# Kernel tuning notes

Measured on AMD Instinct MI355X. Metric: run time of the kernel, lower is better.

The kernel has to match this reference:

```python
import jax, jax.numpy as jnp
import numpy as np

G = 20000          # num_genes
B = 256            # batch_size
NNZ = 640000       # sparse adjacency nonzeros (avg degree 32)
K = 2              # PPR iterations
ALPHA = 0.1
NUM_CLASS = 33


def _spmm(rows, cols, vals, x):
    # y = A @ x with A sparse COO [G, G], x dense [G, B]
    return jax.ops.segment_sum(vals[:, None] * x[cols], rows, num_segments=G)


def setup_inputs() -> dict:
    key = jax.random.key(0)
    ks = jax.random.split(key, 18)
    inp = {
        "x_sample": jax.random.normal(ks[0], (B * G,), jnp.float32),
        "x_TF": jax.random.normal(ks[1], (B * G,), jnp.float32),
        "adj_rows": jax.random.randint(ks[2], (NNZ,), 0, G, jnp.int32),
        "adj_cols": jax.random.randint(ks[3], (NNZ,), 0, G, jnp.int32),
        "adj_vals": jax.random.uniform(ks[4], (NNZ,), jnp.float32) / 32.0,
        "adjT_rows": jax.random.randint(ks[5], (NNZ,), 0, G, jnp.int32),
        "adjT_cols": jax.random.randint(ks[6], (NNZ,), 0, G, jnp.int32),
        "adjT_vals": jax.random.uniform(ks[7], (NNZ,), jnp.float32) / 32.0,
        # learned scalar affine params (torch.rand(1))
        "emb_mut": jax.random.uniform(ks[8], (1,), jnp.float32),
        "bias_mut": jax.random.uniform(ks[9], (1,), jnp.float32),
        "emb_exp": jax.random.uniform(ks[10], (1,), jnp.float32),
        "bias_exp": jax.random.uniform(ks[11], (1,), jnp.float32),
        # MLP params (torch Linear layout: W [out, in])
        "W1": jax.random.normal(ks[12], (1024, G), jnp.float32) * (1.0 / np.sqrt(G)),
        "b1": jnp.zeros((1024,), jnp.float32),
        "W2": jax.random.normal(ks[13], (128, 1024), jnp.float32) * (1.0 / 32.0),
        "b2": jnp.zeros((128,), jnp.float32),
        "W3": jax.random.normal(ks[14], (NUM_CLASS, 128), jnp.float32) * (1.0 / np.sqrt(128.0)),
        "b3": jnp.zeros((NUM_CLASS,), jnp.float32),
    }
    return inp


def reference(x_sample, x_TF, adj_rows, adj_cols, adj_vals,
              adjT_rows, adjT_cols, adjT_vals,
              emb_mut, bias_mut, emb_exp, bias_exp,
              W1, b1, W2, b2, W3, b3):
    # scalar affine embedding + relu
    emb_m = jax.nn.relu(emb_mut * x_sample + bias_mut)   # [B*G]
    emb_e = jax.nn.relu(emb_exp * x_TF + bias_exp)       # [B*G]
    xs = emb_m.reshape(B, G).T                            # [G, B]
    xt = emb_e.reshape(B, G).T                            # [G, B]
    hs, ht = xs, xt
    one_m_a = 1.0 - ALPHA
    for _ in range(K):
        xs = _spmm(adj_rows, adj_cols, adj_vals, one_m_a * xs)
        xt = _spmm(adjT_rows, adjT_cols, adjT_vals, one_m_a * xt)
    xs = xs + ALPHA * hs
    xt = xt + ALPHA * ht
    hadamard = (xs * xt).T                                # [B, G]
    h1 = jax.nn.relu(hadamard @ W1.T + b1)                # [B, 1024]
    h2 = jax.nn.relu(h1 @ W2.T + b2)                      # [B, 128]
    return h2 @ W3.T + b3                                 # [B, num_class]
```

## Files before the change

kernel.cpp:

```cpp
#include <hip/hip_runtime.h>
#include <hip/hip_fp16.h>

#define G_   20000
#define B_   256
#define NNZ_ 640000
#define KCH_ 640
#define NZ_  32
#define NBUK 157
#define BCAP 4608
#define EPB  4000

typedef float f4 __attribute__((ext_vector_type(4)));
typedef _Float16 h8 __attribute__((ext_vector_type(8)));

__global__ __launch_bounds__(256) void embed_kernel(
        const float* __restrict__ xsamp, const float* __restrict__ xtf,
        const float* __restrict__ em, const float* __restrict__ bm,
        const float* __restrict__ ee, const float* __restrict__ be,
        __half* __restrict__ X0s, __half* __restrict__ X0t,
        int* __restrict__ cnt) {
    __shared__ float lds[64][65];
    const int t  = threadIdx.x;
    if (blockIdx.x == 0 && blockIdx.y == 0)
        for (int i = t; i < 2 * NBUK; i += 256) cnt[i] = 0;
    const int gb = blockIdx.x * 64, bb = blockIdx.y * 64;
    const float a_m = em[0], c_m = bm[0], a_e = ee[0], c_e = be[0];
    const int gl = t & 63, brow0 = t >> 6;
    const int cl = t & 31, row0  = t >> 5;
    const int g_l = gb + gl;
#pragma unroll
    for (int r = 0; r < 16; r++) {
        int bl = brow0 + r * 4;
        float v = 0.f;
        if (g_l < G_) v = xsamp[(size_t)(bb + bl) * G_ + g_l];
        lds[bl][gl] = fmaxf(a_m * v + c_m, 0.f);
    }
    __syncthreads();
#pragma unroll
    for (int r = 0; r < 8; r++) {
        int gl2 = row0 + r * 8;
        int g = gb + gl2;
        if (g < G_) {
            __half2 hv = __floats2half2_rn(lds[cl * 2][gl2], lds[cl * 2 + 1][gl2]);
            *(__half2*)(X0s + (size_t)g * B_ + bb + cl * 2) = hv;
        }
    }
    __syncthreads();
#pragma unroll
    for (int r = 0; r < 16; r++) {
        int bl = brow0 + r * 4;
        float v = 0.f;
        if (g_l < G_) v = xtf[(size_t)(bb + bl) * G_ + g_l];
        lds[bl][gl] = fmaxf(a_e * v + c_e, 0.f);
    }
    __syncthreads();
#pragma unroll
    for (int r = 0; r < 8; r++) {
        int gl2 = row0 + r * 8;
        int g = gb + gl2;
        if (g < G_) {
            __half2 hv = __floats2half2_rn(lds[cl * 2][gl2], lds[cl * 2 + 1][gl2]);
            *(__half2*)(X0t + (size_t)g * B_ + bb + cl * 2) = hv;
        }
    }
}

__global__ __launch_bounds__(256) void binsort_kernel(
        const int* __restrict__ rA, const int* __restrict__ cA, const float* __restrict__ vA,
        const int* __restrict__ rB, const int* __restrict__ cB, const float* __restrict__ vB,
        int2* __restrict__ metaA, int* __restrict__ cntA,
        int2* __restrict__ metaB, int* __restrict__ cntB) {
    __shared__ int2 stage[EPB];
    __shared__ unsigned char bkid[EPB];
    __shared__ int hist[NBUK], lstart[NBUK], gbase[NBUK];
    const int t = threadIdx.x;
    const int base = blockIdx.x * EPB;
    const int* rows; const int* colsp; const float* valsp; int2* meta; int* cnt;
    if (blockIdx.y == 0) { rows = rA; colsp = cA; valsp = vA; meta = metaA; cnt = cntA; }
    else                 { rows = rB; colsp = cB; valsp = vB; meta = metaB; cnt = cntB; }

    for (int i = t; i < NBUK; i += 256) hist[i] = 0;
    __syncthreads();
    for (int i = t; i < EPB; i += 256)
        atomicAdd(&hist[rows[base + i] >> 7], 1);
    __syncthreads();
    if (t == 0) {
        int s = 0;
        for (int b = 0; b < NBUK; b++) { lstart[b] = s; s += hist[b]; }
    }
    __syncthreads();
    if (t < NBUK) hist[t] = lstart[t];
    __syncthreads();
    for (int i = t; i < EPB; i += 256) {
        int r = rows[base + i];
        int c = colsp[base + i];
        float v = valsp[base + i];
        int b = r >> 7;
        int p = atomicAdd(&hist[b], 1);
        stage[p] = make_int2(((r & 127) << 24) | (c * (B_ * 2)),
                             __float_as_int(0.9f * v));
        bkid[p] = (unsigned char)b;
    }
    __syncthreads();
    if (t < NBUK) gbase[t] = atomicAdd(&cnt[t], hist[t] - lstart[t]);
    __syncthreads();
    for (int i = t; i < EPB; i += 256) {
        int b = bkid[i];
        meta[(size_t)b * BCAP + gbase[b] + (i - lstart[b])] = stage[i];
    }
}

__global__ __launch_bounds__(256) void rowsort_kernel(
        const int2* __restrict__ metaA, const int* __restrict__ cntA,
        int2* __restrict__ sortedA, int* __restrict__ rpA,
        const int2* __restrict__ metaB, const int* __restrict__ cntB,
        int2* __restrict__ sortedB, int* __restrict__ rpB) {
    __shared__ int2 stage[BCAP];
    __shared__ int2 sorted[BCAP];
    __shared__ int carr[NBUK];
    __shared__ int hist[128], lstart[128];
    const int t = threadIdx.x;
    const int buk = blockIdx.x;
    const int2* meta; const int* cnt; int2* outp; int* rp;
    if (blockIdx.y == 0) { meta = metaA; cnt = cntA; outp = sortedA; rp = rpA; }
    else                 { meta = metaB; cnt = cntB; outp = sortedB; rp = rpB; }

    if (t < NBUK) carr[t] = cnt[t];
    if (t < 128) hist[t] = 0;
    __syncthreads();
    int bukStart = 0;
    const int nE = carr[buk];
    for (int b = 0; b < buk; b++) bukStart += carr[b];

    const int2* mp = meta + (size_t)buk * BCAP;
    for (int i = t; i < nE; i += 256) {
        int2 m = mp[i];
        stage[i] = m;
        atomicAdd(&hist[(unsigned)m.x >> 24], 1);
    }
    __syncthreads();
    if (t == 0) {
        int s = 0;
        for (int r = 0; r < 128; r++) { lstart[r] = s; s += hist[r]; }
    }
    __syncthreads();
    if (t < 128) hist[t] = lstart[t];
    __syncthreads();
    for (int i = t; i < nE; i += 256) {
        int2 m = stage[i];
        int r = (unsigned)m.x >> 24;
        int p = atomicAdd(&hist[r], 1);
        sorted[p] = make_int2(m.x & 0xFFFFFF, m.y);
    }
    __syncthreads();
    for (int i = t; i < nE; i += 256)
        outp[bukStart + i] = sorted[i];
    if (t < 128) {
        int g = buk * 128 + t;
        if (g < G_) rp[g] = bukStart + lstart[t];
    }
    if (buk == NBUK - 1 && t == 0) rp[G_] = bukStart + nE;
}

__device__ __forceinline__ void spmm_load8(const int2* __restrict__ mp, int base,
                                           int2* mm) {
#pragma unroll
    for (int j = 0; j < 8; j++) mm[j] = mp[base + j];
}
__device__ __forceinline__ void spmm_proc8(const int2* mm, const char* xb,
        float& a0, float& a1, float& a2, float& a3) {
    uint2 r[8];
#pragma unroll
    for (int j = 0; j < 8; j++) r[j] = *(const uint2*)(xb + mm[j].x);
#pragma unroll
    for (int j = 0; j < 8; j++) {
        float v = __int_as_float(mm[j].y);
        float2 l = __half22float2(*(__half2*)&r[j].x);
        float2 h = __half22float2(*(__half2*)&r[j].y);
        a0 = fmaf(v, l.x, a0); a1 = fmaf(v, l.y, a1);
        a2 = fmaf(v, h.x, a2); a3 = fmaf(v, h.y, a3);
    }
}

__global__ __launch_bounds__(256) void spmm_kernel(
        const int* __restrict__ rpA, const int2* __restrict__ metaA,
        const __half* __restrict__ xinA, __half* __restrict__ xoutA,
        const int* __restrict__ rpB, const int2* __restrict__ metaB,
        const __half* __restrict__ xinB, __half* __restrict__ xoutB) {
    const int bid = blockIdx.x;
    const int isB = bid >= 5000;
    const int idx = isB ? bid - 5000 : bid;
    const int t = threadIdx.x;
    const int wave = t >> 6, lane = t & 63;
    const int g = idx * 4 + wave;
    const int* rp; const int2* meta; const __half* xin; __half* xout;
    if (!isB) { rp = rpA; meta = metaA; xin = xinA; xout = xoutA; }
    else      { rp = rpB; meta = metaB; xin = xinB; xout = xoutB; }
    const int beg = __builtin_amdgcn_readfirstlane(rp[g]);
    const int n   = __builtin_amdgcn_readfirstlane(rp[g + 1]) - beg;
    const int2* mp = meta + beg;
    const char* xb = (const char*)xin + lane * 8;
    float a0 = 0.f, a1 = 0.f, a2 = 0.f, a3 = 0.f;
    const int nb = n >> 3;
    int2 mA[8], mB[8];
    if (nb > 0) spmm_load8(mp, 0, mA);
    int b2 = 0;
    while (b2 < nb) {
        if (b2 + 1 < nb) spmm_load8(mp, (b2 + 1) * 8, mB);
        spmm_proc8(mA, xb, a0, a1, a2, a3);
        b2++;
        if (b2 >= nb) break;
        if (b2 + 1 < nb) spmm_load8(mp, (b2 + 1) * 8, mA);
        spmm_proc8(mB, xb, a0, a1, a2, a3);
        b2++;
    }
    for (int e = nb * 8; e < n; ++e) {
        int2 m = mp[e];
        float v = __int_as_float(m.y);
        uint2 r = *(const uint2*)(xb + m.x);
        float2 l = __half22float2(*(__half2*)&r.x), h = __half22float2(*(__half2*)&r.y);
        a0 = fmaf(v, l.x, a0); a1 = fmaf(v, l.y, a1);
        a2 = fmaf(v, h.x, a2); a3 = fmaf(v, h.y, a3);
    }
    __half2 o0 = __floats2half2_rn(a0, a1);
    __half2 o1 = __floats2half2_rn(a2, a3);
    uint2 ov;
    ov.x = *(unsigned*)&o0;
    ov.y = *(unsigned*)&o1;
    *(uint2*)((char*)xout + (size_t)g * (B_ * 2) + lane * 8) = ov;
}

__global__ __launch_bounds__(256) void combine_kernel(
        const __half* __restrict__ X2s, const __half* __restrict__ X0s,
        const __half* __restrict__ X2t, const __half* __restrict__ X0t,
        __half* __restrict__ hadBK) {
    __shared__ float lds[64][65];
    const int t = threadIdx.x;
    const int gb = blockIdx.x * 64, bb = blockIdx.y * 64;
    const int cl = t & 31, row0 = t >> 5;
#pragma unroll
    for (int r = 0; r < 8; r++) {
        int gl = row0 + r * 8;
        int g = gb + gl;
        float px = 0.f, py = 0.f;
        if (g < G_) {
            size_t idx = (size_t)g * B_ + bb + cl * 2;
            float2 x2s = __half22float2(*(const __half2*)(X2s + idx));
            float2 x0s = __half22float2(*(const __half2*)(X0s + idx));
            float2 x2t = __half22float2(*(const __half2*)(X2t + idx));
            float2 x0t = __half22float2(*(const __half2*)(X0t + idx));
            px = (x2s.x + 0.1f * x0s.x) * (x2t.x + 0.1f * x0t.x);
            py = (x2s.y + 0.1f * x0s.y) * (x2t.y + 0.1f * x0t.y);
        }
        lds[gl][cl * 2]     = px;
        lds[gl][cl * 2 + 1] = py;
    }
    __syncthreads();
#pragma unroll
    for (int r = 0; r < 8; r++) {
        int bl = row0 + r * 8;
        int g0 = gb + cl * 2;
        if (g0 < G_) {
            __half2 hv = __floats2half2_rn(lds[cl * 2][bl], lds[cl * 2 + 1][bl]);
            *(__half2*)(hadBK + (size_t)(bb + bl) * G_ + g0) = hv;
        }
    }
}

__global__ __launch_bounds__(512) void gemm1_kernel(
        const __half* __restrict__ hadBK, const float* __restrict__ W1,
        float* __restrict__ part) {
    __shared__ _Float16 a_lds[2][256][40];
    __shared__ _Float16 b_lds[2][128][40];
    const int t = threadIdx.x;
    const int lane = t & 63, wid = t >> 6;
    const int wm = wid >> 1, wn = wid & 1;
    const int l15 = lane & 15, l4 = lane >> 4;
    const int ob = blockIdx.x * 128;
    const int kb = blockIdx.y * KCH_;
    int kend = kb + KCH_; if (kend > G_) kend = G_;
    const int nsteps = (kend - kb) >> 5;
    const int ar = t >> 1, ah = t & 1;
    const int br = t >> 2, bs = t & 3;
    const _Float16* hadH = (const _Float16*)hadBK;
    const _Float16* asrc = hadH + (size_t)ar * G_ + ah * 16;
    const float*    bsrc = W1 + (size_t)(ob + br) * G_ + bs * 8;
    f4 acc[4][4] = {};
    h8 ra0 = *(const h8*)(asrc + kb);
    h8 ra1 = *(const h8*)(asrc + kb + 8);
    f4 rb0 = *(const f4*)(bsrc + kb);
    f4 rb1 = *(const f4*)(bsrc + kb + 4);
    *(h8*)&a_lds[0][ar][ah * 16]     = ra0;
    *(h8*)&a_lds[0][ar][ah * 16 + 8] = ra1;
    {
        h8 h;
        h[0] = (_Float16)rb0[0]; h[1] = (_Float16)rb0[1];
        h[2] = (_Float16)rb0[2]; h[3] = (_Float16)rb0[3];
        h[4] = (_Float16)rb1[0]; h[5] = (_Float16)rb1[1];
        h[6] = (_Float16)rb1[2]; h[7] = (_Float16)rb1[3];
        *(h8*)&b_lds[0][br][bs * 8] = h;
    }
    __syncthreads();
    int p = 0;
    for (int s = 0; s < nsteps; ++s) {
        if (s + 1 < nsteps) {
            const int k1 = kb + (s + 1) * 32;
            ra0 = *(const h8*)(asrc + k1);
            ra1 = *(const h8*)(asrc + k1 + 8);
            rb0 = *(const f4*)(bsrc + k1);
            rb1 = *(const f4*)(bsrc + k1 + 4);
        }
        h8 af[4], bf[4];
#pragma unroll
        for (int m = 0; m < 4; m++)
            af[m] = *(const h8*)&a_lds[p][wm * 64 + m * 16 + l15][l4 * 8];
#pragma unroll
        for (int n = 0; n < 4; n++)
            bf[n] = *(const h8*)&b_lds[p][wn * 64 + n * 16 + l15][l4 * 8];
#pragma unroll
        for (int m = 0; m < 4; m++)
#pragma unroll
            for (int n = 0; n < 4; n++)
                acc[m][n] = __builtin_amdgcn_mfma_f32_16x16x32_f16(
                    af[m], bf[n], acc[m][n], 0, 0, 0);
        if (s + 1 < nsteps) {
            *(h8*)&a_lds[p ^ 1][ar][ah * 16]     = ra0;
            *(h8*)&a_lds[p ^ 1][ar][ah * 16 + 8] = ra1;
            h8 h;
            h[0] = (_Float16)rb0[0]; h[1] = (_Float16)rb0[1];
            h[2] = (_Float16)rb0[2]; h[3] = (_Float16)rb0[3];
            h[4] = (_Float16)rb1[0]; h[5] = (_Float16)rb1[1];
            h[6] = (_Float16)rb1[2]; h[7] = (_Float16)rb1[3];
            *(h8*)&b_lds[p ^ 1][br][bs * 8] = h;
            __syncthreads();
            p ^= 1;
        }
    }
    const size_t zoff = (size_t)blockIdx.y * (B_ * 1024);
#pragma unroll
    for (int m = 0; m < 4; m++)
#pragma unroll
        for (int n = 0; n < 4; n++)
#pragma unroll
            for (int j = 0; j < 4; j++) {
                int b = wm * 64 + m * 16 + l4 * 4 + j;
                int o = ob + wn * 64 + n * 16 + l15;
                part[zoff + (size_t)b * 1024 + o] = acc[m][n][j];
            }
}

__global__ __launch_bounds__(256) void gemm23_kernel(
        const float* __restrict__ part, const float* __restrict__ b1,
        const float* __restrict__ W2, const float* __restrict__ b2,
        const float* __restrict__ W3, const float* __restrict__ b3,
        float* __restrict__ out) {
    __shared__ float h1row[1024];
    __shared__ float h2p[2][128];
    const int b = blockIdx.x, t = threadIdx.x;
    {
        f4 s = {0.f, 0.f, 0.f, 0.f};
        const float* pb = part + (size_t)b * 1024;
        for (int z = 0; z < NZ_; z++)
            s += ((const f4*)(pb + (size_t)z * 262144))[t];
        s += ((const f4*)b1)[t];
        f4 r;
        r[0] = fmaxf(s[0], 0.f); r[1] = fmaxf(s[1], 0.f);
        r[2] = fmaxf(s[2], 0.f); r[3] = fmaxf(s[3], 0.f);
        ((f4*)h1row)[t] = r;
    }
    __syncthreads();
    {
        const int o = t & 127, hh = t >> 7;
        float acc = 0.f;
        const f4* w  = (const f4*)(W2 + (size_t)o * 1024 + hh * 512);
        const f4* hr = (const f4*)(h1row + hh * 512);
        for (int k = 0; k < 128; k++) {
            f4 wv = w[k], hv = hr[k];
            acc += wv[0] * hv[0] + wv[1] * hv[1] + wv[2] * hv[2] + wv[3] * hv[3];
        }
        h2p[hh][o] = acc;
    }
    __syncthreads();
    if (t < 128) h2p[0][t] = fmaxf(h2p[0][t] + h2p[1][t] + b2[t], 0.f);
    __syncthreads();
    if (t < 33) {
        float acc = b3[t];
        const f4* w  = (const f4*)(W3 + (size_t)t * 128);
        const f4* hv = (const f4*)h2p[0];
#pragma unroll
        for (int k = 0; k < 32; k++) {
            f4 a = w[k], x = hv[k];
            acc += a[0] * x[0] + a[1] * x[1] + a[2] * x[2] + a[3] * x[3];
        }
        out[b * 33 + t] = acc;
    }
}

extern "C" void kernel_launch(void* const* d_in, const int* in_sizes, int n_in,
                              void* d_out, int out_size, void* d_ws, size_t ws_size,
                              hipStream_t stream) {
    const float* x_sample  = (const float*)d_in[0];
    const float* x_TF      = (const float*)d_in[1];
    const int*   adj_rows  = (const int*)d_in[2];
    const int*   adj_cols  = (const int*)d_in[3];
    const float* adj_vals  = (const float*)d_in[4];
    const int*   adjT_rows = (const int*)d_in[5];
    const int*   adjT_cols = (const int*)d_in[6];
    const float* adjT_vals = (const float*)d_in[7];
    const float* emb_mut   = (const float*)d_in[8];
    const float* bias_mut  = (const float*)d_in[9];
    const float* emb_exp   = (const float*)d_in[10];
    const float* bias_exp  = (const float*)d_in[11];
    const float* W1 = (const float*)d_in[12];
    const float* b1 = (const float*)d_in[13];
    const float* W2 = (const float*)d_in[14];
    const float* b2 = (const float*)d_in[15];
    const float* W3 = (const float*)d_in[16];
    const float* b3 = (const float*)d_in[17];
    float* out = (float*)d_out;

    char* w = (char*)d_ws;
    auto alloc = [&](size_t bytes) {
        char* p = w; w += (bytes + 255) & ~(size_t)255; return p;
    };
    __half* X0s = (__half*)alloc(5120000 * 2);
    __half* X1s = (__half*)alloc(5120000 * 2);
    __half* X2s = (__half*)alloc(5120000 * 2);
    __half* X0t = (__half*)alloc(5120000 * 2);
    __half* X1t = (__half*)alloc(5120000 * 2);
    __half* X2t = (__half*)alloc(5120000 * 2);
    float*  part = (float*)alloc((size_t)NZ_ * 262144 * 4);
    int2*   metaA   = (int2*)alloc((size_t)NBUK * BCAP * 8);
    int2*   metaB   = (int2*)alloc((size_t)NBUK * BCAP * 8);
    int2*   sortedA = (int2*)alloc((size_t)(NNZ_ + 128) * 8);
    int2*   sortedB = (int2*)alloc((size_t)(NNZ_ + 128) * 8);
    int*    cnt   = (int*)alloc(2 * NBUK * 4);
    int*    cntA  = cnt;
    int*    cntB  = cnt + NBUK;
    int*    rpA   = (int*)alloc(20001 * 4);
    int*    rpB   = (int*)alloc(20001 * 4);
    __half* hadBK = X1s;

    embed_kernel<<<dim3(313, 4), 256, 0, stream>>>(
        x_sample, x_TF, emb_mut, bias_mut, emb_exp, bias_exp, X0s, X0t, cnt);

    binsort_kernel<<<dim3(160, 2), 256, 0, stream>>>(
        adj_rows, adj_cols, adj_vals, adjT_rows, adjT_cols, adjT_vals,
        metaA, cntA, metaB, cntB);
    rowsort_kernel<<<dim3(NBUK, 2), 256, 0, stream>>>(
        metaA, cntA, sortedA, rpA, metaB, cntB, sortedB, rpB);

    spmm_kernel<<<10000, 256, 0, stream>>>(rpA, sortedA, X0s, X1s,
                                           rpB, sortedB, X0t, X1t);
    spmm_kernel<<<10000, 256, 0, stream>>>(rpA, sortedA, X1s, X2s,
                                           rpB, sortedB, X1t, X2t);

    combine_kernel<<<dim3(313, 4), 256, 0, stream>>>(X2s, X0s, X2t, X0t, hadBK);

    gemm1_kernel<<<dim3(8, NZ_), 512, 0, stream>>>(hadBK, W1, part);
    gemm23_kernel<<<B_, 256, 0, stream>>>(part, b1, W2, b2, W3, b3, out);
}
```

Baseline: 410.0 us.

## Interleave SpMM graph blocks, widen gather batches, remap GEMM1 blocks to XCDs

The SpMM kernel now interleaves blocks of the two graphs (A and B) instead of putting them in contiguous halves. Its inner loop issues 16 independent gathers per batch with 8/4 tails, replacing the double-buffered 8-wide scheme. GEMM1 switches to a 1D grid whose block-index mapping is meant to place blocks sharing a K-chunk of the A tile on the same XCD for L2 reuse. Risks include higher register pressure from 16-wide gathers and losing the metadata prefetch overlap.

```diff
diff --git a/kernel.cpp b/kernel.cpp
--- a/kernel.cpp
+++ b/kernel.cpp
@@ -162,59 +162,76 @@
     if (buk == NBUK - 1 && t == 0) rp[G_] = bukStart + nE;
 }
 
-__device__ __forceinline__ void spmm_load8(const int2* __restrict__ mp, int base,
-                                           int2* mm) {
-#pragma unroll
-    for (int j = 0; j < 8; j++) mm[j] = mp[base + j];
-}
-__device__ __forceinline__ void spmm_proc8(const int2* mm, const char* xb,
-        float& a0, float& a1, float& a2, float& a3) {
-    uint2 r[8];
-#pragma unroll
-    for (int j = 0; j < 8; j++) r[j] = *(const uint2*)(xb + mm[j].x);
-#pragma unroll
-    for (int j = 0; j < 8; j++) {
-        float v = __int_as_float(mm[j].y);
-        float2 l = __half22float2(*(__half2*)&r[j].x);
-        float2 h = __half22float2(*(__half2*)&r[j].y);
-        a0 = fmaf(v, l.x, a0); a1 = fmaf(v, l.y, a1);
-        a2 = fmaf(v, h.x, a2); a3 = fmaf(v, h.y, a3);
-    }
-}
-
 __global__ __launch_bounds__(256) void spmm_kernel(
         const int* __restrict__ rpA, const int2* __restrict__ metaA,
         const __half* __restrict__ xinA, __half* __restrict__ xoutA,
         const int* __restrict__ rpB, const int2* __restrict__ metaB,
         const __half* __restrict__ xinB, __half* __restrict__ xoutB) {
-    const int bid = blockIdx.x;
-    const int isB = bid >= 5000;
-    const int idx = isB ? bid - 5000 : bid;
+    const int bid   = blockIdx.x;
+    const int combo = bid & 1;
     const int t = threadIdx.x;
     const int wave = t >> 6, lane = t & 63;
-    const int g = idx * 4 + wave;
+    const int g = (bid >> 1) * 4 + wave;
     const int* rp; const int2* meta; const __half* xin; __half* xout;
-    if (!isB) { rp = rpA; meta = metaA; xin = xinA; xout = xoutA; }
-    else      { rp = rpB; meta = metaB; xin = xinB; xout = xoutB; }
+    if (combo == 0) { rp = rpA; meta = metaA; xin = xinA; xout = xoutA; }
+    else            { rp = rpB; meta = metaB; xin = xinB; xout = xoutB; }
     const int beg = __builtin_amdgcn_readfirstlane(rp[g]);
     const int n   = __builtin_amdgcn_readfirstlane(rp[g + 1]) - beg;
     const int2* mp = meta + beg;
     const char* xb = (const char*)xin + lane * 8;
     float a0 = 0.f, a1 = 0.f, a2 = 0.f, a3 = 0.f;
-    const int nb = n >> 3;
-    int2 mA[8], mB[8];
-    if (nb > 0) spmm_load8(mp, 0, mA);
-    int b2 = 0;
-    while (b2 < nb) {
-        if (b2 + 1 < nb) spmm_load8(mp, (b2 + 1) * 8, mB);
-        spmm_proc8(mA, xb, a0, a1, a2, a3);
-        b2++;
-        if (b2 >= nb) break;
-        if (b2 + 1 < nb) spmm_load8(mp, (b2 + 1) * 8, mA);
-        spmm_proc8(mB, xb, a0, a1, a2, a3);
-        b2++;
-    }
-    for (int e = nb * 8; e < n; ++e) {
+    int e = 0;
+    for (; e + 16 <= n; e += 16) {
+        int2 m[16];
+        uint2 r[16];
+#pragma unroll
+        for (int j = 0; j < 16; j++) m[j] = mp[e + j];
+#pragma unroll
+        for (int j = 0; j < 16; j++) r[j] = *(const uint2*)(xb + m[j].x);
+#pragma unroll
+        for (int j = 0; j < 16; j++) {
+            float v = __int_as_float(m[j].y);
+            float2 l = __half22float2(*(__half2*)&r[j].x);
+            float2 h = __half22float2(*(__half2*)&r[j].y);
+            a0 = fmaf(v, l.x, a0); a1 = fmaf(v, l.y, a1);
+            a2 = fmaf(v, h.x, a2); a3 = fmaf(v, h.y, a3);
+        }
+    }
+    if (e + 8 <= n) {
+        int2 m[8];
+        uint2 r[8];
+#pragma unroll
+        for (int j = 0; j < 8; j++) m[j] = mp[e + j];
+#pragma unroll
+        for (int j = 0; j < 8; j++) r[j] = *(const uint2*)(xb + m[j].x);
+#pragma unroll
+        for (int j = 0; j < 8; j++) {
+            float v = __int_as_float(m[j].y);
+            float2 l = __half22float2(*(__half2*)&r[j].x);
+            float2 h = __half22float2(*(__half2*)&r[j].y);
+            a0 = fmaf(v, l.x, a0); a1 = fmaf(v, l.y, a1);
+            a2 = fmaf(v, h.x, a2); a3 = fmaf(v, h.y, a3);
+        }
+        e += 8;
+    }
+    if (e + 4 <= n) {
+        int2 m[4];
+        uint2 r[4];
+#pragma unroll
+        for (int j = 0; j < 4; j++) m[j] = mp[e + j];
+#pragma unroll
+        for (int j = 0; j < 4; j++) r[j] = *(const uint2*)(xb + m[j].x);
+#pragma unroll
+        for (int j = 0; j < 4; j++) {
+            float v = __int_as_float(m[j].y);
+            float2 l = __half22float2(*(__half2*)&r[j].x);
+            float2 h = __half22float2(*(__half2*)&r[j].y);
+            a0 = fmaf(v, l.x, a0); a1 = fmaf(v, l.y, a1);
+            a2 = fmaf(v, h.x, a2); a3 = fmaf(v, h.y, a3);
+        }
+        e += 4;
+    }
+    for (; e < n; ++e) {
         int2 m = mp[e];
         float v = __int_as_float(m.y);
         uint2 r = *(const uint2*)(xb + m.x);
@@ -272,12 +289,16 @@
         float* __restrict__ part) {
     __shared__ _Float16 a_lds[2][256][40];
     __shared__ _Float16 b_lds[2][128][40];
+    const int lid = blockIdx.x;
+    const int xcd = lid & 7, jj = lid >> 3;
+    const int zz = xcd + 8 * (jj & 3);
+    const int oo = jj >> 2;
     const int t = threadIdx.x;
     const int lane = t & 63, wid = t >> 6;
     const int wm = wid >> 1, wn = wid & 1;
     const int l15 = lane & 15, l4 = lane >> 4;
-    const int ob = blockIdx.x * 128;
-    const int kb = blockIdx.y * KCH_;
+    const int ob = oo * 128;
+    const int kb = zz * KCH_;
     int kend = kb + KCH_; if (kend > G_) kend = G_;
     const int nsteps = (kend - kb) >> 5;
     const int ar = t >> 1, ah = t & 1;
@@ -336,7 +357,7 @@
             p ^= 1;
         }
     }
-    const size_t zoff = (size_t)blockIdx.y * (B_ * 1024);
+    const size_t zoff = (size_t)zz * (B_ * 1024);
 #pragma unroll
     for (int m = 0; m < 4; m++)
 #pragma unroll
@@ -457,6 +478,6 @@
 
     combine_kernel<<<dim3(313, 4), 256, 0, stream>>>(X2s, X0s, X2t, X0t, hadBK);
 
-    gemm1_kernel<<<dim3(8, NZ_), 512, 0, stream>>>(hadBK, W1, part);
+    gemm1_kernel<<<256, 512, 0, stream>>>(hadBK, W1, part);
     gemm23_kernel<<<B_, 256, 0, stream>>>(part, b1, W2, b2, W3, b3, out);
 }
```

After: 403.6 us. Within noise of the previous version (-1.6%).
